# Optimization experiments

Hardware: AMD Instinct MI355X
Metric: run time of the kernel (lower is better)

Reference implementation:

```python
import jax, jax.numpy as jnp
import numpy as np

BLOCK_SIZE = 256
HEAD_SIZE = 128
BATCH = 512


def setup_inputs() -> dict:
    key = jax.random.key(0)
    ks = jax.random.split(key, 7)
    s = 1.0 / np.sqrt(HEAD_SIZE)
    x = jax.random.normal(ks[0], (BATCH, BLOCK_SIZE, HEAD_SIZE), dtype=jnp.float32)
    Wk = jax.random.uniform(ks[1], (HEAD_SIZE, HEAD_SIZE), jnp.float32, -s, s)
    bk = jax.random.uniform(ks[2], (HEAD_SIZE,), jnp.float32, -s, s)
    Wq = jax.random.uniform(ks[3], (HEAD_SIZE, HEAD_SIZE), jnp.float32, -s, s)
    bq = jax.random.uniform(ks[4], (HEAD_SIZE,), jnp.float32, -s, s)
    Wv = jax.random.uniform(ks[5], (HEAD_SIZE, HEAD_SIZE), jnp.float32, -s, s)
    bv = jax.random.uniform(ks[6], (HEAD_SIZE,), jnp.float32, -s, s)
    return {"x": x, "Wk": Wk, "bk": bk, "Wq": Wq, "bq": bq, "Wv": Wv, "bv": bv}


def reference(x, Wk, bk, Wq, bq, Wv, bv):
    # Linear layers: y = x @ W.T + b (torch nn.Linear convention)
    k = jnp.einsum('bsd,ed->bse', x, Wk) + bk  # [B,T,H]
    q = jnp.einsum('bsd,ed->bse', x, Wq) + bq
    v = jnp.einsum('bsd,ed->bse', x, Wv) + bv
    # NOTE: original module has NO 1/sqrt(d) scaling — keep faithful.
    scores = jnp.einsum('bqd,bkd->bqk', q, k)  # [B,T,T]
    T = x.shape[1]
    causal = jnp.tril(jnp.ones((T, T), dtype=bool))
    scores = jnp.where(causal, scores, -jnp.inf)
    probs = jax.nn.softmax(scores, axis=-1)
    out = jnp.einsum('bqk,bkd->bqd', probs, v)
    return out
```

## Files before the change

kernel.cpp:

```cpp
#include <hip/hip_runtime.h>
#include <hip/hip_fp16.h>

#define TT 256
#define DD 128
#define NEG -30000.0f

typedef __attribute__((ext_vector_type(4))) float f32x4;
typedef __attribute__((ext_vector_type(8))) _Float16 f16x8;
typedef unsigned int u32;
typedef __attribute__((ext_vector_type(4))) u32 u32x4;
typedef unsigned short u16;

__device__ __forceinline__ u16 tof16(float v) {
  return __builtin_bit_cast(u16, (_Float16)v);
}
__device__ __forceinline__ u32 pkf16(float lo, float hi) {
  return (u32)tof16(lo) | ((u32)tof16(hi) << 16);
}
__device__ __forceinline__ f32x4 mfma16(f16x8 a, f16x8 b, f32x4 c) {
  return __builtin_amdgcn_mfma_f32_16x16x32_f16(a, b, c, 0, 0, 0);
}

template<int P>
__device__ __forceinline__ void convN(const f32x4* src, u32x4* dst, int l15, int g) {
  #pragma unroll
  for (int p = 0; p < P; ++p) {
    u32 p00 = pkf16(src[2*p][0], src[2*p][1]);
    u32 p01 = pkf16(src[2*p][2], src[2*p][3]);
    u32 p10 = pkf16(src[2*p+1][0], src[2*p+1][1]);
    u32 p11 = pkf16(src[2*p+1][2], src[2*p+1][3]);
    u32x4 w;
    #pragma unroll
    for (int wd = 0; wd < 4; ++wd) {
      int srcl = l15 + 16*((2*g + (wd >> 1)) & 3);
      u32 lo = (u32)__shfl((int)((wd & 1) ? p01 : p00), srcl, 64);
      u32 hi = (u32)__shfl((int)((wd & 1) ? p11 : p10), srcl, 64);
      w[wd] = (g >> 1) ? hi : lo;
    }
    dst[p] = w;
  }
}

__global__ void precompute_k(const float* __restrict__ Wk, const float* __restrict__ Wq,
                             const float* __restrict__ bq, const float* __restrict__ Wv,
                             u16* __restrict__ MT, u16* __restrict__ WvB, float* __restrict__ m0) {
  int dp = blockIdx.x;
  int d  = threadIdx.x;
  float acc = 0.f;
  for (int e = 0; e < DD; ++e) acc = fmaf(Wq[e*DD + d], Wk[e*DD + dp], acc);
  MT[dp*DD + d] = tof16(acc);
  WvB[dp*DD + d] = tof16(Wv[dp*DD + d]);
  if (dp == 0) {
    float a0 = 0.f;
    for (int e = 0; e < DD; ++e) a0 = fmaf(bq[e], Wk[e*DD + d], a0);
    m0[d] = a0;
  }
}

__global__ __launch_bounds__(1024, 4)
void head_fused(const float* __restrict__ x, const u16* __restrict__ MTg,
                const u16* __restrict__ WvB, const float* __restrict__ m0g,
                const float* __restrict__ bvg, float* __restrict__ out) {
  extern __shared__ char lds[];
  char* xhb = lds;
  char* vtb = lds + 65536;

  const int tid  = threadIdx.x;
  const int w    = tid >> 6;
  const int lane = tid & 63;
  const int l15  = lane & 15;
  const int g    = lane >> 4;
  const int b    = blockIdx.x;
  const float* xb = x + (size_t)b * (TT*DD);

  int xoff[4];
  #pragma unroll
  for (int kc = 0; kc < 4; ++kc)
    xoff[kc] = kc*1024 + g*256 + (l15 ^ (kc*4 + g))*16;
  const int voff = g*256 + l15*16;

  #pragma unroll
  for (int i = 0; i < 4; ++i) {
    int slot = tid + i*1024;
    int row = slot >> 4, cg = slot & 15;
    const float* p = xb + row*DD + cg*8;
    f32x4 v0 = *(const f32x4*)p, v1 = *(const f32x4*)(p + 4);
    u32x4 pk;
    pk[0] = pkf16(v0[0], v0[1]); pk[1] = pkf16(v0[2], v0[3]);
    pk[2] = pkf16(v1[0], v1[1]); pk[3] = pkf16(v1[2], v1[3]);
    *(u32x4*)(xhb + (row >> 4)*4096 + (cg >> 2)*1024 + (cg & 3)*256
                  + ((row & 15) ^ cg)*16) = pk;
  }
  __syncthreads();

  {
    const int c = w & 7, eh = w >> 3;
    f16x8 bX[2][4];
    #pragma unroll
    for (int t = 0; t < 2; ++t)
      #pragma unroll
      for (int kc = 0; kc < 4; ++kc)
        bX[t][kc] = *(const f16x8*)(xhb + (2*c + t)*4096 + xoff[kc]);
    #pragma unroll
    for (int e = 0; e < 4; ++e) {
      const int et = eh*4 + e;
      f16x8 bWv[4];
      #pragma unroll
      for (int kc = 0; kc < 4; ++kc)
        bWv[kc] = *(const f16x8*)(WvB + (et*16 + l15)*DD + kc*32 + g*8);
      f32x4 vacc[2];
      #pragma unroll
      for (int t = 0; t < 2; ++t) {
        f32x4 acc = {0.f, 0.f, 0.f, 0.f};
        #pragma unroll
        for (int kc = 0; kc < 4; ++kc) acc = mfma16(bX[t][kc], bWv[kc], acc);
        vacc[t] = acc;
      }
      u32x4 dv[1];
      convN<1>(vacc, dv, l15, g);
      *(u32x4*)(vtb + et*8192 + c*1024 + voff) = dv[0];
    }
  }

  const int qt = w;
  u32x4 bAw[4];
  {
    f16x8 bXq[4];
    #pragma unroll
    for (int kc = 0; kc < 4; ++kc)
      bXq[kc] = *(const f16x8*)(xhb + qt*4096 + xoff[kc]);
    f32x4 Aacc[8];
    #pragma unroll
    for (int dt = 0; dt < 8; ++dt) {
      f32x4 acc = {0.f, 0.f, 0.f, 0.f};
      #pragma unroll
      for (int kc = 0; kc < 4; ++kc) {
        f16x8 aM = *(const f16x8*)(MTg + (dt*16 + l15)*DD + kc*32 + g*8);
        acc = mfma16(aM, bXq[kc], acc);
      }
      f32x4 m0v = *(const f32x4*)(m0g + dt*16 + g*4);
      #pragma unroll
      for (int j = 0; j < 4; ++j) acc[j] += m0v[j];
      Aacc[dt] = acc;
    }
    convN<4>(Aacc, bAw, l15, g);
  }
  __syncthreads();

  const int nch = (qt + 2) >> 1;
  f32x4 oacc[8];
  #pragma unroll
  for (int et = 0; et < 8; ++et) { f32x4 z = {0.f,0.f,0.f,0.f}; oacc[et] = z; }
  float m = NEG, sum = 0.f;

  #pragma unroll 1
  for (int c = 0; c < nch; ++c) {
    const int kt0 = 2*c, kt1 = 2*c + 1;
    f32x4 s0 = {0.f, 0.f, 0.f, 0.f};
    f32x4 s1 = {NEG, NEG, NEG, NEG};
    #pragma unroll
    for (int kc = 0; kc < 4; ++kc) {
      f16x8 aX = *(const f16x8*)(xhb + kt0*4096 + xoff[kc]);
      s0 = mfma16(aX, __builtin_bit_cast(f16x8, bAw[kc]), s0);
    }
    if (kt0 == qt) {
      #pragma unroll
      for (int j = 0; j < 4; ++j)
        if (g*4 + j > l15) s0[j] = NEG;
    }
    if (kt1 <= qt) {
      f32x4 acc = {0.f, 0.f, 0.f, 0.f};
      #pragma unroll
      for (int kc = 0; kc < 4; ++kc) {
        f16x8 aX = *(const f16x8*)(xhb + kt1*4096 + xoff[kc]);
        acc = mfma16(aX, __builtin_bit_cast(f16x8, bAw[kc]), acc);
      }
      if (kt1 == qt) {
        #pragma unroll
        for (int j = 0; j < 4; ++j)
          if (g*4 + j > l15) acc[j] = NEG;
      }
      s1 = acc;
    }
    float pmax = NEG;
    #pragma unroll
    for (int j = 0; j < 4; ++j) pmax = fmaxf(pmax, fmaxf(s0[j], s1[j]));
    pmax = fmaxf(pmax, __shfl_xor(pmax, 16));
    pmax = fmaxf(pmax, __shfl_xor(pmax, 32));
    if (!__all(pmax <= m + 8.f)) {
      float mn = fmaxf(m, pmax);
      float f  = __expf(m - mn);
      sum *= f;
      #pragma unroll
      for (int et = 0; et < 8; ++et) {
        #pragma unroll
        for (int j = 0; j < 4; ++j) oacc[et][j] *= f;
      }
      m = mn;
    }
    #pragma unroll
    for (int j = 0; j < 4; ++j) {
      float p0 = __expf(s0[j] - m); s0[j] = p0; sum += p0;
      float p1 = __expf(s1[j] - m); s1[j] = p1; sum += p1;
    }
    u32 p00 = pkf16(s0[0], s0[1]);
    u32 p01 = pkf16(s0[2], s0[3]);
    u32 p10 = pkf16(s1[0], s1[1]);
    u32 p11 = pkf16(s1[2], s1[3]);
    u32x4 pw;
    #pragma unroll
    for (int wd = 0; wd < 4; ++wd) {
      int srcl = l15 + 16*((2*g + (wd >> 1)) & 3);
      u32 lo = (u32)__shfl((int)((wd & 1) ? p01 : p00), srcl, 64);
      u32 hi = (u32)__shfl((int)((wd & 1) ? p11 : p10), srcl, 64);
      pw[wd] = (g >> 1) ? hi : lo;
    }
    f16x8 pb = __builtin_bit_cast(f16x8, pw);
    #pragma unroll
    for (int et = 0; et < 8; ++et) {
      f16x8 aV = *(const f16x8*)(vtb + et*8192 + c*1024 + voff);
      oacc[et] = mfma16(aV, pb, oacc[et]);
    }
  }

  sum += __shfl_xor(sum, 16);
  sum += __shfl_xor(sum, 32);
  const float inv = 1.f / sum;
  float* outb = out + (size_t)b * (TT*DD);
  #pragma unroll
  for (int et = 0; et < 8; ++et) {
    f32x4 bvv = *(const f32x4*)(bvg + et*16 + g*4);
    f32x4 o;
    #pragma unroll
    for (int j = 0; j < 4; ++j) o[j] = oacc[et][j]*inv + bvv[j];
    *(f32x4*)(outb + (qt*16 + l15)*DD + et*16 + g*4) = o;
  }
}

extern "C" void kernel_launch(void* const* d_in, const int* in_sizes, int n_in,
                              void* d_out, int out_size, void* d_ws, size_t ws_size,
                              hipStream_t stream) {
  (void)in_sizes; (void)n_in; (void)out_size; (void)ws_size;
  const float* x  = (const float*)d_in[0];
  const float* Wk = (const float*)d_in[1];
  const float* Wq = (const float*)d_in[3];
  const float* bq = (const float*)d_in[4];
  const float* Wv = (const float*)d_in[5];
  const float* bv = (const float*)d_in[6];

  char* ws = (char*)d_ws;
  u16*   MT  = (u16*)ws;
  u16*   WvB = (u16*)(ws + 32768);
  float* m0  = (float*)(ws + 65536);

  (void)hipFuncSetAttribute((const void*)head_fused,
                            hipFuncAttributeMaxDynamicSharedMemorySize, 131072);

  precompute_k<<<128, 128, 0, stream>>>(Wk, Wq, bq, Wv, MT, WvB, m0);
  head_fused<<<512, 1024, 131072, stream>>>(x, MT, WvB, m0, bv, (float*)d_out);
}
```

Baseline: 92.37 us.

## Balance causal attention work across waves with split-KV merge and exp2 softmax

```diff
diff --git a/kernel.cpp b/kernel.cpp
--- a/kernel.cpp
+++ b/kernel.cpp
@@ -4,6 +4,8 @@
 #define TT 256
 #define DD 128
 #define NEG -30000.0f
+#define LOG2E 1.44269504088896340736f
+#define THR2 11.5416f
 
 typedef __attribute__((ext_vector_type(4))) float f32x4;
 typedef __attribute__((ext_vector_type(8))) _Float16 f16x8;
@@ -48,12 +50,12 @@
   int d  = threadIdx.x;
   float acc = 0.f;
   for (int e = 0; e < DD; ++e) acc = fmaf(Wq[e*DD + d], Wk[e*DD + dp], acc);
-  MT[dp*DD + d] = tof16(acc);
+  MT[dp*DD + d] = tof16(acc * LOG2E);
   WvB[dp*DD + d] = tof16(Wv[dp*DD + d]);
   if (dp == 0) {
     float a0 = 0.f;
     for (int e = 0; e < DD; ++e) a0 = fmaf(bq[e], Wk[e*DD + d], a0);
-    m0[d] = a0;
+    m0[d] = a0 * LOG2E;
   }
 }
 
@@ -121,119 +123,179 @@
       *(u32x4*)(vtb + et*8192 + c*1024 + voff) = dv[0];
     }
   }
-
-  const int qt = w;
-  u32x4 bAw[4];
-  {
-    f16x8 bXq[4];
-    #pragma unroll
-    for (int kc = 0; kc < 4; ++kc)
-      bXq[kc] = *(const f16x8*)(xhb + qt*4096 + xoff[kc]);
-    f32x4 Aacc[8];
-    #pragma unroll
-    for (int dt = 0; dt < 8; ++dt) {
-      f32x4 acc = {0.f, 0.f, 0.f, 0.f};
+  __syncthreads();
+
+  int solo = -1;
+  if (w & 1) { if (w <= 11) solo = 7 - (w >> 1); }
+  else if (w <= 2) solo = 1 - (w >> 1);
+  const int half = w & 1;
+  const int tsp  = 8 + (w >> 1);
+  const int nchS = (tsp + 2) >> 1;
+  const int hS   = (nchS + 1) >> 1;
+
+  float m = NEG, sum = 0.f;
+  f32x4 oacc[8];
+  float* outb = out + (size_t)b * (TT*DD);
+
+  #pragma unroll 1
+  for (int a = 0; a < 2; ++a) {
+    int qt, c0, c1;
+    if (a == 0) {
+      if (solo < 0) continue;
+      qt = solo; c0 = 0; c1 = (solo + 2) >> 1;
+    } else {
+      qt = tsp; c0 = half ? hS : 0; c1 = half ? nchS : hS;
+    }
+    u32x4 bAw[4];
+    {
+      f16x8 bXq[4];
+      #pragma unroll
+      for (int kc = 0; kc < 4; ++kc)
+        bXq[kc] = *(const f16x8*)(xhb + qt*4096 + xoff[kc]);
+      f32x4 Aacc[8];
+      #pragma unroll
+      for (int dt = 0; dt < 8; ++dt) {
+        f32x4 acc = {0.f, 0.f, 0.f, 0.f};
+        #pragma unroll
+        for (int kc = 0; kc < 4; ++kc) {
+          f16x8 aM = *(const f16x8*)(MTg + (dt*16 + l15)*DD + kc*32 + g*8);
+          acc = mfma16(aM, bXq[kc], acc);
+        }
+        f32x4 m0v = *(const f32x4*)(m0g + dt*16 + g*4);
+        #pragma unroll
+        for (int j = 0; j < 4; ++j) acc[j] += m0v[j];
+        Aacc[dt] = acc;
+      }
+      convN<4>(Aacc, bAw, l15, g);
+    }
+    m = NEG; sum = 0.f;
+    #pragma unroll
+    for (int et = 0; et < 8; ++et) { f32x4 z = {0.f,0.f,0.f,0.f}; oacc[et] = z; }
+
+    #pragma unroll 1
+    for (int c = c0; c < c1; ++c) {
+      const int kt0 = 2*c, kt1 = 2*c + 1;
+      f32x4 s0 = {0.f, 0.f, 0.f, 0.f};
+      f32x4 s1 = {NEG, NEG, NEG, NEG};
       #pragma unroll
       for (int kc = 0; kc < 4; ++kc) {
-        f16x8 aM = *(const f16x8*)(MTg + (dt*16 + l15)*DD + kc*32 + g*8);
-        acc = mfma16(aM, bXq[kc], acc);
-      }
-      f32x4 m0v = *(const f32x4*)(m0g + dt*16 + g*4);
-      #pragma unroll
-      for (int j = 0; j < 4; ++j) acc[j] += m0v[j];
-      Aacc[dt] = acc;
-    }
-    convN<4>(Aacc, bAw, l15, g);
-  }
-  __syncthreads();
-
-  const int nch = (qt + 2) >> 1;
-  f32x4 oacc[8];
-  #pragma unroll
-  for (int et = 0; et < 8; ++et) { f32x4 z = {0.f,0.f,0.f,0.f}; oacc[et] = z; }
-  float m = NEG, sum = 0.f;
-
-  #pragma unroll 1
-  for (int c = 0; c < nch; ++c) {
-    const int kt0 = 2*c, kt1 = 2*c + 1;
-    f32x4 s0 = {0.f, 0.f, 0.f, 0.f};
-    f32x4 s1 = {NEG, NEG, NEG, NEG};
-    #pragma unroll
-    for (int kc = 0; kc < 4; ++kc) {
-      f16x8 aX = *(const f16x8*)(xhb + kt0*4096 + xoff[kc]);
-      s0 = mfma16(aX, __builtin_bit_cast(f16x8, bAw[kc]), s0);
-    }
-    if (kt0 == qt) {
-      #pragma unroll
-      for (int j = 0; j < 4; ++j)
-        if (g*4 + j > l15) s0[j] = NEG;
-    }
-    if (kt1 <= qt) {
-      f32x4 acc = {0.f, 0.f, 0.f, 0.f};
-      #pragma unroll
-      for (int kc = 0; kc < 4; ++kc) {
-        f16x8 aX = *(const f16x8*)(xhb + kt1*4096 + xoff[kc]);
-        acc = mfma16(aX, __builtin_bit_cast(f16x8, bAw[kc]), acc);
-      }
-      if (kt1 == qt) {
+        f16x8 aX = *(const f16x8*)(xhb + kt0*4096 + xoff[kc]);
+        s0 = mfma16(aX, __builtin_bit_cast(f16x8, bAw[kc]), s0);
+      }
+      if (kt0 == qt) {
         #pragma unroll
         for (int j = 0; j < 4; ++j)
-          if (g*4 + j > l15) acc[j] = NEG;
-      }
-      s1 = acc;
-    }
-    float pmax = NEG;
-    #pragma unroll
-    for (int j = 0; j < 4; ++j) pmax = fmaxf(pmax, fmaxf(s0[j], s1[j]));
-    pmax = fmaxf(pmax, __shfl_xor(pmax, 16));
-    pmax = fmaxf(pmax, __shfl_xor(pmax, 32));
-    if (!__all(pmax <= m + 8.f)) {
-      float mn = fmaxf(m, pmax);
-      float f  = __expf(m - mn);
-      sum *= f;
+          if (g*4 + j > l15) s0[j] = NEG;
+      }
+      if (kt1 <= qt) {
+        f32x4 acc = {0.f, 0.f, 0.f, 0.f};
+        #pragma unroll
+        for (int kc = 0; kc < 4; ++kc) {
+          f16x8 aX = *(const f16x8*)(xhb + kt1*4096 + xoff[kc]);
+          acc = mfma16(aX, __builtin_bit_cast(f16x8, bAw[kc]), acc);
+        }
+        if (kt1 == qt) {
+          #pragma unroll
+          for (int j = 0; j < 4; ++j)
+            if (g*4 + j > l15) acc[j] = NEG;
+        }
+        s1 = acc;
+      }
+      float pmax = NEG;
+      #pragma unroll
+      for (int j = 0; j < 4; ++j) pmax = fmaxf(pmax, fmaxf(s0[j], s1[j]));
+      pmax = fmaxf(pmax, __shfl_xor(pmax, 16));
+      pmax = fmaxf(pmax, __shfl_xor(pmax, 32));
+      if (!__all(pmax <= m + THR2)) {
+        float mn = fmaxf(m, pmax);
+        float f  = exp2f(m - mn);
+        sum *= f;
+        #pragma unroll
+        for (int et = 0; et < 8; ++et) {
+          #pragma unroll
+          for (int j = 0; j < 4; ++j) oacc[et][j] *= f;
+        }
+        m = mn;
+      }
+      #pragma unroll
+      for (int j = 0; j < 4; ++j) {
+        float p0 = exp2f(s0[j] - m); s0[j] = p0; sum += p0;
+        float p1 = exp2f(s1[j] - m); s1[j] = p1; sum += p1;
+      }
+      u32 p00 = pkf16(s0[0], s0[1]);
+      u32 p01 = pkf16(s0[2], s0[3]);
+      u32 p10 = pkf16(s1[0], s1[1]);
+      u32 p11 = pkf16(s1[2], s1[3]);
+      u32x4 pw;
+      #pragma unroll
+      for (int wd = 0; wd < 4; ++wd) {
+        int srcl = l15 + 16*((2*g + (wd >> 1)) & 3);
+        u32 lo = (u32)__shfl((int)((wd & 1) ? p01 : p00), srcl, 64);
+        u32 hi = (u32)__shfl((int)((wd & 1) ? p11 : p10), srcl, 64);
+        pw[wd] = (g >> 1) ? hi : lo;
+      }
+      f16x8 pb = __builtin_bit_cast(f16x8, pw);
       #pragma unroll
       for (int et = 0; et < 8; ++et) {
-        #pragma unroll
-        for (int j = 0; j < 4; ++j) oacc[et][j] *= f;
-      }
-      m = mn;
-    }
-    #pragma unroll
-    for (int j = 0; j < 4; ++j) {
-      float p0 = __expf(s0[j] - m); s0[j] = p0; sum += p0;
-      float p1 = __expf(s1[j] - m); s1[j] = p1; sum += p1;
-    }
-    u32 p00 = pkf16(s0[0], s0[1]);
-    u32 p01 = pkf16(s0[2], s0[3]);
-    u32 p10 = pkf16(s1[0], s1[1]);
-    u32 p11 = pkf16(s1[2], s1[3]);
-    u32x4 pw;
-    #pragma unroll
-    for (int wd = 0; wd < 4; ++wd) {
-      int srcl = l15 + 16*((2*g + (wd >> 1)) & 3);
-      u32 lo = (u32)__shfl((int)((wd & 1) ? p01 : p00), srcl, 64);
-      u32 hi = (u32)__shfl((int)((wd & 1) ? p11 : p10), srcl, 64);
-      pw[wd] = (g >> 1) ? hi : lo;
-    }
-    f16x8 pb = __builtin_bit_cast(f16x8, pw);
-    #pragma unroll
-    for (int et = 0; et < 8; ++et) {
-      f16x8 aV = *(const f16x8*)(vtb + et*8192 + c*1024 + voff);
-      oacc[et] = mfma16(aV, pb, oacc[et]);
+        f16x8 aV = *(const f16x8*)(vtb + et*8192 + c*1024 + voff);
+        oacc[et] = mfma16(aV, pb, oacc[et]);
+      }
+    }
+
+    if (a == 0) {
+      float s = sum;
+      s += __shfl_xor(s, 16);
+      s += __shfl_xor(s, 32);
+      const float inv = 1.f / s;
+      #pragma unroll
+      for (int et = 0; et < 8; ++et) {
+        f32x4 bvv = *(const f32x4*)(bvg + et*16 + g*4);
+        f32x4 o;
+        #pragma unroll
+        for (int j = 0; j < 4; ++j) o[j] = oacc[et][j]*inv + bvv[j];
+        *(f32x4*)(outb + (qt*16 + l15)*DD + et*16 + g*4) = o;
+      }
     }
   }
 
   sum += __shfl_xor(sum, 16);
   sum += __shfl_xor(sum, 32);
-  const float inv = 1.f / sum;
-  float* outb = out + (size_t)b * (TT*DD);
-  #pragma unroll
-  for (int et = 0; et < 8; ++et) {
-    f32x4 bvv = *(const f32x4*)(bvg + et*16 + g*4);
-    f32x4 o;
-    #pragma unroll
-    for (int j = 0; j < 4; ++j) o[j] = oacc[et][j]*inv + bvv[j];
-    *(f32x4*)(outb + (qt*16 + l15)*DD + et*16 + g*4) = o;
+  __syncthreads();
+  float* msum = (float*)(lds + 65536);
+  if (g == 0) {
+    msum[((w >> 1)*2 + half)*32 + l15]      = m;
+    msum[((w >> 1)*2 + half)*32 + 16 + l15] = sum;
+  }
+  __syncthreads();
+  const float mo = msum[((w >> 1)*2 + (half ^ 1))*32 + l15];
+  const float so = msum[((w >> 1)*2 + (half ^ 1))*32 + 16 + l15];
+  const float ms = fmaxf(m, mo);
+  const float fs = exp2f(m - ms);
+  const float fo = exp2f(mo - ms);
+  const float stot = sum*fs + so*fo;
+  float* oex = (float*)lds;
+  if (!half) {
+    #pragma unroll
+    for (int et = 0; et < 8; ++et) {
+      f32x4 o;
+      #pragma unroll
+      for (int j = 0; j < 4; ++j) o[j] = oacc[et][j]*fs;
+      *(f32x4*)(oex + (w >> 1)*2048 + et*256 + lane*4) = o;
+    }
+  }
+  __syncthreads();
+  if (half) {
+    const float inv = 1.f / stot;
+    #pragma unroll
+    for (int et = 0; et < 8; ++et) {
+      f32x4 pe = *(const f32x4*)(oex + (w >> 1)*2048 + et*256 + lane*4);
+      f32x4 bvv = *(const f32x4*)(bvg + et*16 + g*4);
+      f32x4 o;
+      #pragma unroll
+      for (int j = 0; j < 4; ++j)
+        o[j] = (pe[j] + oacc[et][j]*fs) * inv + bvv[j];
+      *(f32x4*)(outb + (tsp*16 + l15)*DD + et*16 + g*4) = o;
+    }
   }
 }
 
```

Result: slower. 141.0 us (+52.7%).
